# Kernel tuning notes

Measured on AMD Instinct MI355X. Metric: run time of the kernel, lower is better.

The kernel has to match this reference:

```python
import jax, jax.numpy as jnp
import numpy as np

N_NODES = 20000
N_EDGES = 320000
N_FEAT = 128
N_CLASS = 10
NEG_SLOPE = 0.2  # PyG GATConv default LeakyReLU slope


def gat_conv(x, src, dst, ew, W, a_src, a_dst, b, heads, ch, concat):
    """PyG-style GATConv with multiplicative edge_weight on messages.
    x: [N, Fin]; src/dst: [E] (self-loops already included); ew: [E].
    """
    N = x.shape[0]
    h = (x @ W).reshape(N, heads, ch)                      # [N,H,C]
    al_s = jnp.sum(h * a_src, axis=-1)                     # [N,H]
    al_d = jnp.sum(h * a_dst, axis=-1)                     # [N,H]
    e = jax.nn.leaky_relu(al_s[src] + al_d[dst], NEG_SLOPE)  # [E,H]
    # segment softmax over incoming edges of each target node
    m = jax.ops.segment_max(e, dst, num_segments=N)        # [N,H]
    ex = jnp.exp(e - m[dst])
    den = jax.ops.segment_sum(ex, dst, num_segments=N)     # [N,H]
    alpha = ex / (den[dst] + 1e-16)                        # [E,H]
    msg = h[src] * (alpha * ew[:, None])[..., None]        # [E,H,C]
    out = jax.ops.segment_sum(msg, dst, num_segments=N)    # [N,H,C]
    out = out.reshape(N, heads * ch) if concat else out.mean(axis=1)
    return out + b


def setup_inputs() -> dict:
    key = jax.random.key(0)
    ks = jax.random.split(key, 20)
    d = {}
    d["x"] = jax.random.normal(ks[0], (N_NODES, N_FEAT), dtype=jnp.float32)
    d["edge_index"] = jax.random.randint(ks[1], (2, N_EDGES), 0, N_NODES, dtype=jnp.int32)
    d["edge_weight"] = jnp.ones((N_EDGES,), dtype=jnp.float32)

    def glorot(k, shape):
        fan = shape[0] + shape[-1]
        return jax.random.uniform(k, shape, jnp.float32, -1.0, 1.0) * np.sqrt(6.0 / fan)

    H1, C1 = 4, 256
    H3, C3 = 6, N_CLASS
    d["W1"] = glorot(ks[2], (N_FEAT, H1 * C1))
    d["a1s"] = glorot(ks[3], (H1, C1)) * 0.1
    d["a1d"] = glorot(ks[4], (H1, C1)) * 0.1
    d["b1"] = jnp.zeros((H1 * C1,), jnp.float32)
    d["lw1"] = glorot(ks[5], (N_FEAT, H1 * C1))
    d["lb1"] = jnp.zeros((H1 * C1,), jnp.float32)

    d["W2"] = glorot(ks[6], (H1 * C1, H1 * C1))
    d["a2s"] = glorot(ks[7], (H1, C1)) * 0.1
    d["a2d"] = glorot(ks[8], (H1, C1)) * 0.1
    d["b2"] = jnp.zeros((H1 * C1,), jnp.float32)
    d["lw2"] = glorot(ks[9], (H1 * C1, H1 * C1))
    d["lb2"] = jnp.zeros((H1 * C1,), jnp.float32)

    d["W3"] = glorot(ks[10], (H1 * C1, H3 * C3))
    d["a3s"] = glorot(ks[11], (H3, C3)) * 0.1
    d["a3d"] = glorot(ks[12], (H3, C3)) * 0.1
    d["b3"] = jnp.zeros((C3,), jnp.float32)
    d["lw3"] = glorot(ks[13], (H1 * C1, C3))
    d["lb3"] = jnp.zeros((C3,), jnp.float32)
    return d


def reference(x, edge_index, edge_weight,
              W1, a1s, a1d, b1, lw1, lb1,
              W2, a2s, a2d, b2, lw2, lb2,
              W3, a3s, a3d, b3, lw3, lb3):
    N = x.shape[0]
    # PyG GATConv adds self-loops (fill edge_weight with 1.0)
    loop = jnp.arange(N, dtype=edge_index.dtype)
    src = jnp.concatenate([edge_index[0], loop])
    dst = jnp.concatenate([edge_index[1], loop])
    ew = jnp.concatenate([edge_weight, jnp.ones((N,), edge_weight.dtype)])

    h = jax.nn.elu(gat_conv(x, src, dst, ew, W1, a1s, a1d, b1, 4, 256, True)
                   + (x @ lw1 + lb1))
    h = jax.nn.elu(gat_conv(h, src, dst, ew, W2, a2s, a2d, b2, 4, 256, True)
                   + (h @ lw2 + lb2))
    out = gat_conv(h, src, dst, ew, W3, a3s, a3d, b3, 6, N_CLASS, False) \
          + (h @ lw3 + lb3)
    return out
```

## Files before the change

### kernel.cpp

```cpp
#include <hip/hip_runtime.h>

typedef __attribute__((ext_vector_type(8))) short s16x8;
typedef __attribute__((ext_vector_type(8))) __bf16 bf16x8;
typedef __attribute__((ext_vector_type(4))) float f32x4;

__device__ inline float bf2f(ushort u){ return __uint_as_float(((unsigned)u)<<16); }
__device__ inline ushort f2bf(float f){
  unsigned u = __float_as_uint(f);
  unsigned r = (u + 0x7fffu + ((u>>16)&1u)) >> 16;
  return (ushort)r;
}

__device__ inline void gl_lds16(const ushort* g, ushort* l){
  __builtin_amdgcn_global_load_lds(
      (const __attribute__((address_space(1))) unsigned int*)g,
      (__attribute__((address_space(3))) unsigned int*)l,
      16, 0, 0);
}

__global__ void k_count(const int* __restrict__ ei, int* __restrict__ counts,
                        int E, int ET){
  int e = blockIdx.x*256 + threadIdx.x;
  if (e >= ET) return;
  int dst = (e < E) ? ei[E + e] : (e - E);
  atomicAdd(&counts[dst], 1);
}

__global__ __launch_bounds__(1024) void k_scan(const int* __restrict__ cnt,
                                               int* __restrict__ indptr, int N){
  __shared__ int part[1024];
  int t = threadIdx.x;
  int per = (N + 1023) / 1024;
  int base = t * per;
  int s = 0;
  for (int i = 0; i < per; ++i){ int idx = base + i; if (idx < N) s += cnt[idx]; }
  part[t] = s; __syncthreads();
  for (int off = 1; off < 1024; off <<= 1){
    int v = (t >= off) ? part[t-off] : 0;
    __syncthreads();
    if (t >= off) part[t] += v;
    __syncthreads();
  }
  int run = (t == 0) ? 0 : part[t-1];
  for (int i = 0; i < per; ++i){
    int idx = base + i;
    if (idx < N){ indptr[idx] = run; run += cnt[idx]; }
  }
  if (t == 1023) indptr[N] = run;
}

__global__ void k_fill(const int* __restrict__ ei, const float* __restrict__ ew,
                       const int* __restrict__ indptr, int* __restrict__ cursor,
                       int* __restrict__ csrc, float* __restrict__ cew,
                       int E, int ET){
  int e = blockIdx.x*256 + threadIdx.x;
  if (e >= ET) return;
  int src, dst; float w;
  if (e < E){ src = ei[e]; dst = ei[E + e]; w = ew[e]; }
  else { src = dst = e - E; w = 1.0f; }
  int pos = indptr[dst] + atomicAdd(&cursor[dst], 1);
  csrc[pos] = src; cew[pos] = w;
}

__global__ void k_f2b(const float* __restrict__ x, ushort* __restrict__ xb,
                      int n8valid, int n8total){
  int i = blockIdx.x*256 + threadIdx.x;
  if (i >= n8total) return;
  s16x8 o = {0,0,0,0,0,0,0,0};
  if (i < n8valid){
    const float4* p = (const float4*)x + (size_t)i*2;
    float4 a = p[0], b = p[1];
    o[0]=(short)f2bf(a.x); o[1]=(short)f2bf(a.y); o[2]=(short)f2bf(a.z); o[3]=(short)f2bf(a.w);
    o[4]=(short)f2bf(b.x); o[5]=(short)f2bf(b.y); o[6]=(short)f2bf(b.z); o[7]=(short)f2bf(b.w);
  }
  *((s16x8*)xb + i) = o;
}

__global__ __launch_bounds__(256) void k_packB(
    const float* __restrict__ W, const float* __restrict__ LW,
    ushort* __restrict__ BT, int K, int NW, int NL, int Npad)
{
  __shared__ float tile[32][33];
  int k0 = blockIdx.x*32, n0 = blockIdx.y*32;
  int c = threadIdx.x & 31, r4 = threadIdx.x >> 5;
  #pragma unroll
  for (int rr = 0; rr < 32; rr += 8){
    int k = k0 + r4 + rr, n = n0 + c;
    float v = 0.f;
    if (k < K){
      if (n < NW)            v = W[(size_t)k*NW + n];
      else if (n < NW + NL)  v = LW[(size_t)k*NL + (n - NW)];
    }
    tile[r4+rr][c] = v;
  }
  __syncthreads();
  #pragma unroll
  for (int rr = 0; rr < 32; rr += 8){
    int n = n0 + r4 + rr, k = k0 + c;
    if (n < Npad && k < K) BT[(size_t)n*K + k] = f2bf(tile[c][r4+rr]);
  }
}

__global__ __launch_bounds__(256) void k_gemm(
    const ushort* __restrict__ A, const ushort* __restrict__ BT,
    ushort* __restrict__ Gatt, ushort* __restrict__ Skip,
    int K, int GW, int SW, int NCB, int CPX)
{
  __shared__ ushort As[128*64];
  __shared__ ushort Bs[128*64];
  const int bid = blockIdx.x;
  const int lb = CPX ? ((bid & 7)*CPX + (bid >> 3)) : bid;
  const size_t row0 = (size_t)(lb / NCB) * 128;
  const size_t col0 = (size_t)(lb % NCB) * 128;
  const int t = threadIdx.x;
  const int l = t & 63, w = t >> 6;
  const int wr = w >> 1, wc = w & 1;
  const int sr = l >> 3;
  const int sk = ((l & 7) ^ sr) << 3;
  const ushort* gA = A  + (row0 + w*8 + sr)*(size_t)K + sk;
  const ushort* gB = BT + (col0 + w*8 + sr)*(size_t)K + sk;
  ushort* lA = As + w*512;
  ushort* lB = Bs + w*512;
  const int rf = l & 15;
  const int g4 = l >> 4;
  f32x4 acc[4][4] = {};

  for (int k0 = 0; k0 < K; k0 += 64){
    #pragma unroll
    for (int i = 0; i < 4; ++i){
      gl_lds16(gA + k0 + (size_t)(i*32)*K, lA + i*2048);
      gl_lds16(gB + k0 + (size_t)(i*32)*K, lB + i*2048);
    }
    __syncthreads();
    #pragma unroll
    for (int kk = 0; kk < 2; ++kk){
      const int koff = ((((kk<<2) | g4) ^ (rf & 7)) << 3);
      bf16x8 af[4], bfr[4];
      #pragma unroll
      for (int i = 0; i < 4; ++i)
        af[i] = __builtin_bit_cast(bf16x8, *(const s16x8*)(As + (wr*64 + i*16 + rf)*64 + koff));
      #pragma unroll
      for (int j = 0; j < 4; ++j)
        bfr[j] = __builtin_bit_cast(bf16x8, *(const s16x8*)(Bs + (wc*64 + j*16 + rf)*64 + koff));
      #pragma unroll
      for (int i = 0; i < 4; ++i)
        #pragma unroll
        for (int j = 0; j < 4; ++j)
          acc[i][j] = __builtin_amdgcn_mfma_f32_16x16x32_bf16(af[i], bfr[j], acc[i][j], 0, 0, 0);
    }
    __syncthreads();
  }

  #pragma unroll
  for (int i = 0; i < 4; ++i){
    #pragma unroll
    for (int j = 0; j < 4; ++j){
      int gc = (int)col0 + wc*64 + j*16 + rf;
      #pragma unroll
      for (int r = 0; r < 4; ++r){
        size_t gr = row0 + wr*64 + i*16 + (g4<<2) + r;
        float v = acc[i][j][r];
        if (gc < GW)            Gatt[gr*GW + gc] = f2bf(v);
        else if (gc < GW + SW)  Skip[gr*SW + (gc - GW)] = f2bf(v);
      }
    }
  }
}

#define STG8(p0, hh, ktv, offU) do { \
  const ushort* _g = (p0) + (((size_t)(hh))<<7)*(size_t)K + (((size_t)(ktv))<<6); \
  gl_lds16(_g, S + (offU) + (w<<9)); \
  gl_lds16(_g + ((size_t)K<<6), S + (offU) + 4096 + (w<<9)); \
} while(0)

#define RD_A(base_) do { _Pragma("unroll") \
  for (int i_ = 0; i_ < 4; ++i_){ \
    const int hr = wr*64 + i_*16 + rf; const int sw = hr & 7; \
    av[i_][0] = *(const bf16x8*)((base_) + hr*64 + ((g4 ^ sw) << 3)); \
    av[i_][1] = *(const bf16x8*)((base_) + hr*64 + (((4|g4) ^ sw) << 3)); } \
} while(0)

#define RD_B(base_, dst_) do { _Pragma("unroll") \
  for (int j_ = 0; j_ < 2; ++j_){ \
    const int cf = wc*32 + j_*16 + rf; const int sw = cf & 7; \
    dst_[j_][0] = *(const bf16x8*)((base_) + cf*64 + ((g4 ^ sw) << 3)); \
    dst_[j_][1] = *(const bf16x8*)((base_) + cf*64 + (((4|g4) ^ sw) << 3)); } \
} while(0)

#define MM8(mh, nh, bv_) do { \
  __builtin_amdgcn_s_setprio(1); \
  _Pragma("unroll") \
  for (int kk_ = 0; kk_ < 2; ++kk_) \
    _Pragma("unroll") \
    for (int i_ = 0; i_ < 4; ++i_) \
      _Pragma("unroll") \
      for (int j_ = 0; j_ < 2; ++j_) \
        acc[mh][nh][i_][j_] = __builtin_amdgcn_mfma_f32_16x16x32_bf16( \
            av[i_][kk_], bv_[j_][kk_], acc[mh][nh][i_][j_], 0, 0, 0); \
  __builtin_amdgcn_s_setprio(0); \
} while(0)

__global__ __launch_bounds__(512, 1) void k_gemm8(
    const ushort* __restrict__ A, const ushort* __restrict__ BT,
    ushort* __restrict__ Gatt, ushort* __restrict__ Skip,
    int K, int GW, int CPX)
{
  __shared__ ushort S[65536];
  const int bid = blockIdx.x;
  const int lb = (bid & 7)*CPX + (bid >> 3);
  const size_t row0 = (size_t)(lb >> 3) * 256;
  const size_t col0 = (size_t)(lb & 7) * 256;
  const int t = threadIdx.x;
  const int l = t & 63, w = t >> 6;
  const int wr = w >> 2, wc = w & 3;
  const int rf = l & 15, g4 = l >> 4;
  const int T = K >> 6;

  const int r0 = t >> 3, s0 = t & 7;
  const ushort* pA = A  + (row0 + r0)*(size_t)K + ((s0 ^ (r0 & 7)) << 3);
  const ushort* pB = BT + (col0 + r0)*(size_t)K + ((s0 ^ (r0 & 7)) << 3);

  f32x4 acc[2][2][4][2] = {};
  bf16x8 av[4][2], bvlo[2][2], bvhi[2][2];

  STG8(pA, 0, 0, 0);
  STG8(pB, 0, 0, 16384);
  STG8(pA, 1, 0, 8192);
  STG8(pB, 1, 0, 24576);
  STG8(pA, 0, 1, 32768);
  STG8(pB, 0, 1, 49152);
  asm volatile("s_waitcnt vmcnt(4)");
  asm volatile("s_barrier" ::: "memory");

  for (int u = 0; u < T; ++u){
    const int b = u & 1;
    const int bbase = b << 15;
    const int nbase = bbase ^ 32768;
    const bool un1 = (u + 1 < T), un2 = (u + 2 < T);
    const ushort* Alo = S + bbase;
    const ushort* Ahi = S + bbase + 8192;
    const ushort* Blo = S + bbase + 16384;
    const ushort* Bhi = S + bbase + 24576;
    RD_A(Alo); RD_B(Blo, bvlo);
    if (un1) STG8(pA, 1, u+1, nbase + 8192);
    MM8(0, 0, bvlo);
    asm volatile("s_barrier" ::: "memory");
    RD_B(Bhi, bvhi);
    if (un1) STG8(pB, 1, u+1, nbase + 24576);
    MM8(0, 1, bvhi);
    asm volatile("s_barrier" ::: "memory");
    RD_A(Ahi);
    if (un2) STG8(pA, 0, u+2, bbase);
    MM8(1, 1, bvhi);
    asm volatile("s_barrier" ::: "memory");
    if (un2) STG8(pB, 0, u+2, bbase + 16384);
    MM8(1, 0, bvlo);
    if (un2) asm volatile("s_waitcnt vmcnt(4)");
    else     asm volatile("s_waitcnt vmcnt(0)");
    asm volatile("s_barrier" ::: "memory");
  }

  ushort* outp; int cb;
  if ((int)col0 < GW){ outp = Gatt; cb = (int)col0; }
  else               { outp = Skip; cb = (int)col0 - GW; }
  #pragma unroll
  for (int mh = 0; mh < 2; ++mh)
    #pragma unroll
    for (int i = 0; i < 4; ++i)
      #pragma unroll
      for (int rr = 0; rr < 4; ++rr){
        size_t gr = row0 + mh*128 + wr*64 + i*16 + (g4<<2) + rr;
        ushort* rp = outp + gr*1024 + cb;
        #pragma unroll
        for (int nh = 0; nh < 2; ++nh)
          #pragma unroll
          for (int j = 0; j < 2; ++j)
            rp[nh*128 + wc*32 + j*16 + rf] = f2bf(acc[mh][nh][i][j][rr]);
      }
}

__global__ __launch_bounds__(256) void k_al(const ushort* __restrict__ Gatt,
    const float* __restrict__ a_s, const float* __restrict__ a_d,
    float* __restrict__ als, float* __restrict__ ald, int N){
  int gw = (blockIdx.x*blockDim.x + threadIdx.x) >> 6;
  int l = threadIdx.x & 63;
  if (gw >= N) return;
  const ushort* row = Gatt + (size_t)gw*1024;
  int c0 = l*16;
  s16x8 v0 = *(const s16x8*)(row + c0);
  s16x8 v1 = *(const s16x8*)(row + c0 + 8);
  float ps = 0.f, pd = 0.f;
  #pragma unroll
  for (int q = 0; q < 8; ++q){
    float f0 = bf2f((ushort)v0[q]), f1 = bf2f((ushort)v1[q]);
    ps += f0*a_s[c0+q] + f1*a_s[c0+8+q];
    pd += f0*a_d[c0+q] + f1*a_d[c0+8+q];
  }
  #pragma unroll
  for (int off = 8; off; off >>= 1){
    ps += __shfl_down(ps, off);
    pd += __shfl_down(pd, off);
  }
  if ((l & 15) == 0){
    als[(size_t)gw*4 + (l>>4)] = ps;
    ald[(size_t)gw*4 + (l>>4)] = pd;
  }
}

__global__ __launch_bounds__(256) void k_agg(
    const ushort* __restrict__ Gatt,
    const ushort* __restrict__ Skip,
    const float*  __restrict__ als,
    const float*  __restrict__ ald,
    const float*  __restrict__ bias,
    const float*  __restrict__ lbias,
    const int*    __restrict__ indptr,
    const int*    __restrict__ csrc,
    const float*  __restrict__ cew,
    ushort* __restrict__ Hout,
    int N)
{
  const int t = threadIdx.x;
  const int l = t & 63, w = t >> 6;
  const int n = blockIdx.x*4 + w;
  const int h2 = l >> 4;
  const int col = l*16;
  if (n >= N){
    s16x8 z = {0,0,0,0,0,0,0,0};
    *(s16x8*)(Hout + (size_t)n*1024 + col)     = z;
    *(s16x8*)(Hout + (size_t)n*1024 + col + 8) = z;
    return;
  }
  const int beg = indptr[n];
  const int deg = indptr[n+1] - beg;
  const int hh = l & 3;
  const float aldh = ald[(size_t)n*4 + hh];

  float m = -1e30f, d = 0.f;
  for (int c0 = 0; c0 < deg; c0 += 16){
    int i = c0 + (l >> 2);
    bool act = (i < deg);
    float e = -1e30f;
    if (act){
      int s = csrc[beg + i];
      float r_ = als[(size_t)s*4 + hh] + aldh;
      e = r_ > 0.f ? r_ : 0.2f*r_;
    }
    float cm = e;
    #pragma unroll
    for (int o = 4; o < 64; o <<= 1) cm = fmaxf(cm, __shfl_xor(cm, o));
    float nm = fmaxf(m, cm);
    float ex = act ? __expf(e - nm) : 0.f;
    #pragma unroll
    for (int o = 4; o < 64; o <<= 1) ex += __shfl_xor(ex, o);
    d = d * __expf(m - nm) + ex;
    m = nm;
  }
  d += 1e-16f;
  const float inv_d = 1.0f / d;

  float a[16];
  #pragma unroll
  for (int q = 0; q < 16; ++q) a[q] = 0.f;
  const ushort* gbase = Gatt + col;
  for (int c0 = 0; c0 < deg; c0 += 16){
    int i = c0 + (l >> 2);
    int nc = min(16, deg - c0);
    float wv = 0.f; int sv = 0;
    if (i < deg){
      sv = csrc[beg + i];
      float r_ = als[(size_t)sv*4 + hh] + aldh;
      float e = r_ > 0.f ? r_ : 0.2f*r_;
      wv = __expf(e - m) * inv_d * cew[beg + i];
    }
    for (int jj = 0; jj < nc; ++jj){
      float wg = __shfl(wv, (jj << 2) | h2);
      int s    = __shfl(sv, jj << 2);
      const ushort* rp = gbase + (size_t)s*1024;
      s16x8 h0 = *(const s16x8*)rp;
      s16x8 h1 = *(const s16x8*)(rp + 8);
      #pragma unroll
      for (int q = 0; q < 8; ++q) a[q]   += wg * bf2f((ushort)h0[q]);
      #pragma unroll
      for (int q = 0; q < 8; ++q) a[q+8] += wg * bf2f((ushort)h1[q]);
    }
  }

  s16x8 sk0 = *(const s16x8*)(Skip + (size_t)n*1024 + col);
  s16x8 sk1 = *(const s16x8*)(Skip + (size_t)n*1024 + col + 8);
  s16x8 ov0, ov1;
  #pragma unroll
  for (int q = 0; q < 8; ++q){
    float v = a[q] + bias[col+q] + lbias[col+q] + bf2f((ushort)sk0[q]);
    v = v > 0.f ? v : __expf(v) - 1.f;
    ov0[q] = (short)f2bf(v);
    float v2 = a[q+8] + bias[col+8+q] + lbias[col+8+q] + bf2f((ushort)sk1[q]);
    v2 = v2 > 0.f ? v2 : __expf(v2) - 1.f;
    ov1[q] = (short)f2bf(v2);
  }
  *(s16x8*)(Hout + (size_t)n*1024 + col)     = ov0;
  *(s16x8*)(Hout + (size_t)n*1024 + col + 8) = ov1;
}

__global__ void k_al3(const ushort* __restrict__ G3, const float* __restrict__ a_s,
                      const float* __restrict__ a_d,
                      float* __restrict__ als, float* __restrict__ ald, int N){
  int n = blockIdx.x*256 + threadIdx.x;
  if (n >= N) return;
  const ushort* row = G3 + (size_t)n*60;
  #pragma unroll
  for (int h = 0; h < 6; ++h){
    float ps = 0.f, pd = 0.f;
    #pragma unroll
    for (int c = 0; c < 10; ++c){
      float v = bf2f(row[h*10 + c]);
      ps += v * a_s[h*10 + c];
      pd += v * a_d[h*10 + c];
    }
    als[(size_t)n*6 + h] = ps;
    ald[(size_t)n*6 + h] = pd;
  }
}

__global__ __launch_bounds__(64) void k_agg3(
    const ushort* __restrict__ G3,
    const ushort* __restrict__ Skip3,
    const float*  __restrict__ als,
    const float*  __restrict__ ald,
    const float*  __restrict__ b3,
    const float*  __restrict__ lb3,
    const int*    __restrict__ indptr,
    const int*    __restrict__ csrc,
    const float*  __restrict__ cew,
    float* __restrict__ out, int N)
{
  const int n = blockIdx.x;
  const int l = threadIdx.x;
  const int beg = indptr[n], deg = indptr[n+1] - beg;
  __shared__ float s_aldh[6];
  __shared__ int   s_src[64];
  __shared__ float s_wgt[64][6];
  __shared__ float s_o[6][10];
  if (l < 6) s_aldh[l] = ald[(size_t)n*6 + l];
  __syncthreads();
  float m0=-1e30f,m1=-1e30f,m2=-1e30f,m3=-1e30f,m4=-1e30f,m5=-1e30f;
  float d0=0.f,d1=0.f,d2=0.f,d3=0.f,d4=0.f,d5=0.f;
  for (int c0 = 0; c0 < deg; c0 += 64){
    int nc = min(64, deg - c0);
    bool act = l < nc;
    int s = act ? csrc[beg + c0 + l] : 0;
#define HP(hh, mm, dd) { \
    float e = -1e30f; \
    if (act){ float r_ = als[(size_t)s*6 + hh] + s_aldh[hh]; e = r_ > 0.f ? r_ : 0.2f*r_; } \
    float cm = e; \
    for (int o_ = 32; o_; o_ >>= 1) cm = fmaxf(cm, __shfl_xor(cm, o_)); \
    float nm = fmaxf(mm, cm); \
    float ex = act ? __expf(e - nm) : 0.f; \
    for (int o_ = 32; o_; o_ >>= 1) ex += __shfl_xor(ex, o_); \
    dd = dd * __expf(mm - nm) + ex; mm = nm; }
    HP(0,m0,d0) HP(1,m1,d1) HP(2,m2,d2) HP(3,m3,d3) HP(4,m4,d4) HP(5,m5,d5)
#undef HP
  }
  const int h = l / 10, c = l % 10;
  float o = 0.f;
  for (int c0 = 0; c0 < deg; c0 += 64){
    int nc = min(64, deg - c0);
    if (l < nc){
      int s = csrc[beg + c0 + l];
      s_src[l] = s;
      float w_ = cew[beg + c0 + l];
#define WP(hh, mm, dd) { \
      float r_ = als[(size_t)s*6 + hh] + s_aldh[hh]; \
      float e = r_ > 0.f ? r_ : 0.2f*r_; \
      s_wgt[l][hh] = __expf(e - mm) / (dd + 1e-16f) * w_; }
      WP(0,m0,d0) WP(1,m1,d1) WP(2,m2,d2) WP(3,m3,d3) WP(4,m4,d4) WP(5,m5,d5)
#undef WP
    }
    __syncthreads();
    if (l < 60){
      for (int i = 0; i < nc; ++i)
        o += s_wgt[i][h] * bf2f(G3[(size_t)s_src[i]*60 + l]);
    }
    __syncthreads();
  }
  if (l < 60) s_o[h][c] = o;
  __syncthreads();
  if (l < 10){
    float v = (s_o[0][l]+s_o[1][l]+s_o[2][l]+s_o[3][l]+s_o[4][l]+s_o[5][l]) * (1.0f/6.0f);
    v += b3[l] + lb3[l] + bf2f(Skip3[(size_t)n*10 + l]);
    out[(size_t)n*10 + l] = v;
  }
}

extern "C" void kernel_launch(void* const* d_in, const int* in_sizes, int n_in,
                              void* d_out, int out_size, void* d_ws, size_t ws_size,
                              hipStream_t stream)
{
  const int N = 20000, F = 128, E = 320000, ET = E + N;
  const int Mpad = 20224;
  const int F1 = 1024, NT = 2048;
  const int NWG1 = (Mpad/128)*(NT/128);
  const int NWG2 = (Mpad/256)*(NT/256);

  const float* x   = (const float*)d_in[0];
  const int*   ei  = (const int*)  d_in[1];
  const float* ew  = (const float*)d_in[2];
  const float* W1  = (const float*)d_in[3];
  const float* a1s = (const float*)d_in[4];
  const float* a1d = (const float*)d_in[5];
  const float* b1  = (const float*)d_in[6];
  const float* lw1 = (const float*)d_in[7];
  const float* lb1 = (const float*)d_in[8];
  const float* W2  = (const float*)d_in[9];
  const float* a2s = (const float*)d_in[10];
  const float* a2d = (const float*)d_in[11];
  const float* b2  = (const float*)d_in[12];
  const float* lw2 = (const float*)d_in[13];
  const float* lb2 = (const float*)d_in[14];
  const float* W3  = (const float*)d_in[15];
  const float* a3s = (const float*)d_in[16];
  const float* a3d = (const float*)d_in[17];
  const float* b3  = (const float*)d_in[18];
  const float* lw3 = (const float*)d_in[19];
  const float* lb3 = (const float*)d_in[20];

  char* ws = (char*)d_ws;
  size_t off = 0;
  auto alloc = [&](size_t bytes) -> void* {
    void* p = ws + off;
    off = (off + bytes + 255) & ~(size_t)255;
    return p;
  };
  ushort* Gatt = (ushort*)alloc((size_t)Mpad*F1*2);
  ushort* Skip = (ushort*)alloc((size_t)Mpad*F1*2);
  ushort* H    = (ushort*)alloc((size_t)Mpad*F1*2);
  ushort* xb   = (ushort*)alloc((size_t)Mpad*F*2);
  ushort* BT   = (ushort*)alloc((size_t)NT*1024*2);
  float*  als  = (float*) alloc((size_t)N*6*4);
  float*  ald  = (float*) alloc((size_t)N*6*4);
  int*    counts = (int*)alloc((size_t)2*N*4);
  int*    cursor = counts + N;
  int*    indptr = (int*)alloc((size_t)(N+1)*4);
  int*    csrc   = (int*)alloc((size_t)ET*4);
  float*  cew    = (float*)alloc((size_t)ET*4);
  if (off > ws_size) return;

  hipMemsetAsync(counts, 0, (size_t)2*N*4, stream);
  k_count<<<(ET+255)/256, 256, 0, stream>>>(ei, counts, E, ET);
  k_scan<<<1, 1024, 0, stream>>>(counts, indptr, N);
  k_fill<<<(ET+255)/256, 256, 0, stream>>>(ei, ew, indptr, cursor, csrc, cew, E, ET);
  k_f2b<<<(Mpad*F/8+255)/256, 256, 0, stream>>>(x, xb, N*F/8, Mpad*F/8);

  k_packB<<<dim3((F+31)/32, NT/32), 256, 0, stream>>>(W1, lw1, BT, F, 1024, 1024, NT);
  k_gemm<<<dim3(NWG1), 256, 0, stream>>>(xb, BT, Gatt, Skip, F, 1024, 1024, NT/128, NWG1/8);
  k_al<<<(N+3)/4, 256, 0, stream>>>(Gatt, a1s, a1d, als, ald, N);
  k_agg<<<Mpad/4, 256, 0, stream>>>(Gatt, Skip, als, ald, b1, lb1, indptr, csrc, cew, H, N);

  k_packB<<<dim3(F1/32, NT/32), 256, 0, stream>>>(W2, lw2, BT, F1, 1024, 1024, NT);
  k_gemm8<<<dim3(NWG2), 512, 0, stream>>>(H, BT, Gatt, Skip, F1, 1024, NWG2/8);
  k_al<<<(N+3)/4, 256, 0, stream>>>(Gatt, a2s, a2d, als, ald, N);
  k_agg<<<Mpad/4, 256, 0, stream>>>(Gatt, Skip, als, ald, b2, lb2, indptr, csrc, cew, H, N);

  k_packB<<<dim3(F1/32, 128/32), 256, 0, stream>>>(W3, lw3, BT, F1, 60, 10, 128);
  k_gemm<<<dim3(Mpad/128), 256, 0, stream>>>(H, BT, Gatt, Skip, F1, 60, 10, 1, 0);
  k_al3<<<(N+255)/256, 256, 0, stream>>>(Gatt, a3s, a3d, als, ald, N);
  k_agg3<<<N, 64, 0, stream>>>(Gatt, Skip, als, ald, b3, lb3, indptr, csrc, cew,
                               (float*)d_out, N);
}
```

Measured before the change: 501.6 us.

## Merge prep kernels, batch weight packing, split-K layer-3 GEMM, unroll aggregation

Folds the edge-count and x-to-bf16 conversion into one launch, and packs all three weight matrices in a single launch into separate buffers. Layer 1 now runs on the large-tile k_gemm8 kernel (K=128) instead of the small-tile GEMM. The narrow layer-3 GEMM is split four ways along K into fp32 partials that a new reduction kernel sums. The k_gemm8 main loop is peeled so the final two steps carry no conditionals, and the aggregation gather handles two neighbours per iteration for more loads in flight. The cost is an extra fp32 partial buffer and reduction pass, plus possible poor fit of the 256-tile GEMM at K=128 (only two K steps).

After: 480.7 us. 1.04x faster.

```diff
diff --git a/kernel.cpp b/kernel.cpp
--- a/kernel.cpp
+++ b/kernel.cpp
@@ -18,12 +18,27 @@
       16, 0, 0);
 }
 
-__global__ void k_count(const int* __restrict__ ei, int* __restrict__ counts,
-                        int E, int ET){
-  int e = blockIdx.x*256 + threadIdx.x;
-  if (e >= ET) return;
-  int dst = (e < E) ? ei[E + e] : (e - E);
-  atomicAdd(&counts[dst], 1);
+__global__ void k_prep(const int* __restrict__ ei, int* __restrict__ counts,
+                       const float* __restrict__ x, ushort* __restrict__ xb,
+                       int E, int ET, int ETb, int n8valid, int n8total){
+  int b = blockIdx.x;
+  if (b < ETb){
+    int e = b*256 + threadIdx.x;
+    if (e >= ET) return;
+    int dst = (e < E) ? ei[E + e] : (e - E);
+    atomicAdd(&counts[dst], 1);
+  } else {
+    int i = (b - ETb)*256 + threadIdx.x;
+    if (i >= n8total) return;
+    s16x8 o = {0,0,0,0,0,0,0,0};
+    if (i < n8valid){
+      const float4* p = (const float4*)x + (size_t)i*2;
+      float4 a = p[0], bb = p[1];
+      o[0]=(short)f2bf(a.x); o[1]=(short)f2bf(a.y); o[2]=(short)f2bf(a.z); o[3]=(short)f2bf(a.w);
+      o[4]=(short)f2bf(bb.x); o[5]=(short)f2bf(bb.y); o[6]=(short)f2bf(bb.z); o[7]=(short)f2bf(bb.w);
+    }
+    *((s16x8*)xb + i) = o;
+  }
 }
 
 __global__ __launch_bounds__(1024) void k_scan(const int* __restrict__ cnt,
@@ -62,26 +77,18 @@
   csrc[pos] = src; cew[pos] = w;
 }
 
-__global__ void k_f2b(const float* __restrict__ x, ushort* __restrict__ xb,
-                      int n8valid, int n8total){
-  int i = blockIdx.x*256 + threadIdx.x;
-  if (i >= n8total) return;
-  s16x8 o = {0,0,0,0,0,0,0,0};
-  if (i < n8valid){
-    const float4* p = (const float4*)x + (size_t)i*2;
-    float4 a = p[0], b = p[1];
-    o[0]=(short)f2bf(a.x); o[1]=(short)f2bf(a.y); o[2]=(short)f2bf(a.z); o[3]=(short)f2bf(a.w);
-    o[4]=(short)f2bf(b.x); o[5]=(short)f2bf(b.y); o[6]=(short)f2bf(b.z); o[7]=(short)f2bf(b.w);
-  }
-  *((s16x8*)xb + i) = o;
-}
-
-__global__ __launch_bounds__(256) void k_packB(
-    const float* __restrict__ W, const float* __restrict__ LW,
-    ushort* __restrict__ BT, int K, int NW, int NL, int Npad)
+__global__ __launch_bounds__(256) void k_packB3(
+    const float* __restrict__ W1, const float* __restrict__ Lw1, ushort* __restrict__ B1,
+    const float* __restrict__ W2, const float* __restrict__ Lw2, ushort* __restrict__ B2,
+    const float* __restrict__ W3, const float* __restrict__ Lw3, ushort* __restrict__ B3)
 {
   __shared__ float tile[32][33];
-  int k0 = blockIdx.x*32, n0 = blockIdx.y*32;
+  int b = blockIdx.x;
+  const float *W, *L; ushort* B; int K, NW, NL, Np, nkb, lb;
+  if (b < 256)      { W=W1; L=Lw1; B=B1; K=128;  NW=1024; NL=1024; Np=2048; nkb=4;  lb=b; }
+  else if (b < 2304){ W=W2; L=Lw2; B=B2; K=1024; NW=1024; NL=1024; Np=2048; nkb=32; lb=b-256; }
+  else              { W=W3; L=Lw3; B=B3; K=1024; NW=60;   NL=10;   Np=128;  nkb=32; lb=b-2304; }
+  int k0 = (lb % nkb)*32, n0 = (lb / nkb)*32;
   int c = threadIdx.x & 31, r4 = threadIdx.x >> 5;
   #pragma unroll
   for (int rr = 0; rr < 32; rr += 8){
@@ -89,7 +96,7 @@
     float v = 0.f;
     if (k < K){
       if (n < NW)            v = W[(size_t)k*NW + n];
-      else if (n < NW + NL)  v = LW[(size_t)k*NL + (n - NW)];
+      else if (n < NW + NL)  v = L[(size_t)k*NL + (n - NW)];
     }
     tile[r4+rr][c] = v;
   }
@@ -97,35 +104,35 @@
   #pragma unroll
   for (int rr = 0; rr < 32; rr += 8){
     int n = n0 + r4 + rr, k = k0 + c;
-    if (n < Npad && k < K) BT[(size_t)n*K + k] = f2bf(tile[c][r4+rr]);
-  }
-}
-
-__global__ __launch_bounds__(256) void k_gemm(
+    if (n < Np && k < K) B[(size_t)n*K + k] = f2bf(tile[c][r4+rr]);
+  }
+}
+
+__global__ __launch_bounds__(256) void k_gemm_sk(
     const ushort* __restrict__ A, const ushort* __restrict__ BT,
-    ushort* __restrict__ Gatt, ushort* __restrict__ Skip,
-    int K, int GW, int SW, int NCB, int CPX)
+    float* __restrict__ P, int K, int kseg, int Mpad)
 {
   __shared__ ushort As[128*64];
   __shared__ ushort Bs[128*64];
   const int bid = blockIdx.x;
-  const int lb = CPX ? ((bid & 7)*CPX + (bid >> 3)) : bid;
-  const size_t row0 = (size_t)(lb / NCB) * 128;
-  const size_t col0 = (size_t)(lb % NCB) * 128;
+  const int part = bid & 3;
+  const size_t row0 = (size_t)(bid >> 2) * 128;
+  const int kbeg = part * kseg;
+  const int kend = kbeg + kseg;
   const int t = threadIdx.x;
   const int l = t & 63, w = t >> 6;
   const int wr = w >> 1, wc = w & 1;
   const int sr = l >> 3;
   const int sk = ((l & 7) ^ sr) << 3;
   const ushort* gA = A  + (row0 + w*8 + sr)*(size_t)K + sk;
-  const ushort* gB = BT + (col0 + w*8 + sr)*(size_t)K + sk;
+  const ushort* gB = BT + (w*8 + sr)*(size_t)K + sk;
   ushort* lA = As + w*512;
   ushort* lB = Bs + w*512;
   const int rf = l & 15;
   const int g4 = l >> 4;
   f32x4 acc[4][4] = {};
 
-  for (int k0 = 0; k0 < K; k0 += 64){
+  for (int k0 = kbeg; k0 < kend; k0 += 64){
     #pragma unroll
     for (int i = 0; i < 4; ++i){
       gl_lds16(gA + k0 + (size_t)(i*32)*K, lA + i*2048);
@@ -151,20 +158,30 @@
     __syncthreads();
   }
 
+  float* Pp = P + (size_t)part * Mpad * 128;
   #pragma unroll
   for (int i = 0; i < 4; ++i){
     #pragma unroll
     for (int j = 0; j < 4; ++j){
-      int gc = (int)col0 + wc*64 + j*16 + rf;
+      int gc = wc*64 + j*16 + rf;
       #pragma unroll
       for (int r = 0; r < 4; ++r){
         size_t gr = row0 + wr*64 + i*16 + (g4<<2) + r;
-        float v = acc[i][j][r];
-        if (gc < GW)            Gatt[gr*GW + gc] = f2bf(v);
-        else if (gc < GW + SW)  Skip[gr*SW + (gc - GW)] = f2bf(v);
+        Pp[gr*128 + gc] = acc[i][j][r];
       }
     }
   }
+}
+
+__global__ void k_red3(const float* __restrict__ P, ushort* __restrict__ G3,
+                       ushort* __restrict__ S3, int Mpad){
+  int idx = blockIdx.x*256 + threadIdx.x;
+  int row = idx >> 7, gc = idx & 127;
+  if (row >= Mpad || gc >= 70) return;
+  const size_t st = (size_t)Mpad*128;
+  float v = P[idx] + P[idx+st] + P[idx+2*st] + P[idx+3*st];
+  if (gc < 60) G3[(size_t)row*60 + gc] = f2bf(v);
+  else         S3[(size_t)row*10 + (gc-60)] = f2bf(v);
 }
 
 #define STG8(p0, hh, ktv, offU) do { \
@@ -198,6 +215,33 @@
         acc[mh][nh][i_][j_] = __builtin_amdgcn_mfma_f32_16x16x32_bf16( \
             av[i_][kk_], bv_[j_][kk_], acc[mh][nh][i_][j_], 0, 0, 0); \
   __builtin_amdgcn_s_setprio(0); \
+} while(0)
+
+#define KSTEP(u_, UN1, UN2) do { \
+  const int b_ = (u_) & 1; \
+  const int bbase = b_ << 15; \
+  const int nbase = bbase ^ 32768; \
+  const ushort* Alo = S + bbase; \
+  const ushort* Ahi = S + bbase + 8192; \
+  const ushort* Blo = S + bbase + 16384; \
+  const ushort* Bhi = S + bbase + 24576; \
+  RD_A(Alo); RD_B(Blo, bvlo); \
+  if (UN1) STG8(pA, 1, (u_)+1, nbase + 8192); \
+  MM8(0, 0, bvlo); \
+  asm volatile("s_barrier" ::: "memory"); \
+  RD_B(Bhi, bvhi); \
+  if (UN1) STG8(pB, 1, (u_)+1, nbase + 24576); \
+  MM8(0, 1, bvhi); \
+  asm volatile("s_barrier" ::: "memory"); \
+  RD_A(Ahi); \
+  if (UN2) STG8(pA, 0, (u_)+2, bbase); \
+  MM8(1, 1, bvhi); \
+  asm volatile("s_barrier" ::: "memory"); \
+  if (UN2) STG8(pB, 0, (u_)+2, bbase + 16384); \
+  MM8(1, 0, bvlo); \
+  if (UN2) asm volatile("s_waitcnt vmcnt(4)"); \
+  else     asm volatile("s_waitcnt vmcnt(0)"); \
+  asm volatile("s_barrier" ::: "memory"); \
 } while(0)
 
 __global__ __launch_bounds__(512, 1) void k_gemm8(
@@ -232,33 +276,10 @@
   asm volatile("s_waitcnt vmcnt(4)");
   asm volatile("s_barrier" ::: "memory");
 
-  for (int u = 0; u < T; ++u){
-    const int b = u & 1;
-    const int bbase = b << 15;
-    const int nbase = bbase ^ 32768;
-    const bool un1 = (u + 1 < T), un2 = (u + 2 < T);
-    const ushort* Alo = S + bbase;
-    const ushort* Ahi = S + bbase + 8192;
-    const ushort* Blo = S + bbase + 16384;
-    const ushort* Bhi = S + bbase + 24576;
-    RD_A(Alo); RD_B(Blo, bvlo);
-    if (un1) STG8(pA, 1, u+1, nbase + 8192);
-    MM8(0, 0, bvlo);
-    asm volatile("s_barrier" ::: "memory");
-    RD_B(Bhi, bvhi);
-    if (un1) STG8(pB, 1, u+1, nbase + 24576);
-    MM8(0, 1, bvhi);
-    asm volatile("s_barrier" ::: "memory");
-    RD_A(Ahi);
-    if (un2) STG8(pA, 0, u+2, bbase);
-    MM8(1, 1, bvhi);
-    asm volatile("s_barrier" ::: "memory");
-    if (un2) STG8(pB, 0, u+2, bbase + 16384);
-    MM8(1, 0, bvlo);
-    if (un2) asm volatile("s_waitcnt vmcnt(4)");
-    else     asm volatile("s_waitcnt vmcnt(0)");
-    asm volatile("s_barrier" ::: "memory");
-  }
+  int u = 0;
+  for (; u + 2 < T; ++u) KSTEP(u, true, true);
+  KSTEP(u, true, false); ++u;
+  KSTEP(u, false, false);
 
   ushort* outp; int cb;
   if ((int)col0 < GW){ outp = Gatt; cb = (int)col0; }
@@ -373,16 +394,35 @@
       float e = r_ > 0.f ? r_ : 0.2f*r_;
       wv = __expf(e - m) * inv_d * cew[beg + i];
     }
-    for (int jj = 0; jj < nc; ++jj){
+    int jj = 0;
+    for (; jj + 1 < nc; jj += 2){
+      float wg0 = __shfl(wv, (jj << 2) | h2);
+      int   sg0 = __shfl(sv, jj << 2);
+      float wg1 = __shfl(wv, ((jj+1) << 2) | h2);
+      int   sg1 = __shfl(sv, (jj+1) << 2);
+      const ushort* rp0 = gbase + (size_t)sg0*1024;
+      const ushort* rp1 = gbase + (size_t)sg1*1024;
+      s16x8 x0 = *(const s16x8*)rp0;
+      s16x8 x1 = *(const s16x8*)(rp0 + 8);
+      s16x8 y0 = *(const s16x8*)rp1;
+      s16x8 y1 = *(const s16x8*)(rp1 + 8);
+      #pragma unroll
+      for (int q = 0; q < 8; ++q){
+        a[q]   += wg0 * bf2f((ushort)x0[q]) + wg1 * bf2f((ushort)y0[q]);
+        a[q+8] += wg0 * bf2f((ushort)x1[q]) + wg1 * bf2f((ushort)y1[q]);
+      }
+    }
+    if (jj < nc){
       float wg = __shfl(wv, (jj << 2) | h2);
-      int s    = __shfl(sv, jj << 2);
+      int   s  = __shfl(sv, jj << 2);
       const ushort* rp = gbase + (size_t)s*1024;
       s16x8 h0 = *(const s16x8*)rp;
       s16x8 h1 = *(const s16x8*)(rp + 8);
       #pragma unroll
-      for (int q = 0; q < 8; ++q) a[q]   += wg * bf2f((ushort)h0[q]);
-      #pragma unroll
-      for (int q = 0; q < 8; ++q) a[q+8] += wg * bf2f((ushort)h1[q]);
+      for (int q = 0; q < 8; ++q){
+        a[q]   += wg * bf2f((ushort)h0[q]);
+        a[q+8] += wg * bf2f((ushort)h1[q]);
+      }
     }
   }
 
@@ -499,7 +539,6 @@
   const int N = 20000, F = 128, E = 320000, ET = E + N;
   const int Mpad = 20224;
   const int F1 = 1024, NT = 2048;
-  const int NWG1 = (Mpad/128)*(NT/128);
   const int NWG2 = (Mpad/256)*(NT/256);
 
   const float* x   = (const float*)d_in[0];
@@ -535,7 +574,10 @@
   ushort* Skip = (ushort*)alloc((size_t)Mpad*F1*2);
   ushort* H    = (ushort*)alloc((size_t)Mpad*F1*2);
   ushort* xb   = (ushort*)alloc((size_t)Mpad*F*2);
-  ushort* BT   = (ushort*)alloc((size_t)NT*1024*2);
+  ushort* BT1  = (ushort*)alloc((size_t)NT*F*2);
+  ushort* BT2  = (ushort*)alloc((size_t)NT*F1*2);
+  ushort* BT3  = (ushort*)alloc((size_t)128*F1*2);
+  float*  P    = (float*) alloc((size_t)4*Mpad*128*4);
   float*  als  = (float*) alloc((size_t)N*6*4);
   float*  ald  = (float*) alloc((size_t)N*6*4);
   int*    counts = (int*)alloc((size_t)2*N*4);
@@ -545,24 +587,26 @@
   float*  cew    = (float*)alloc((size_t)ET*4);
   if (off > ws_size) return;
 
+  const int ETb = (ET + 255)/256;
+  const int n8tot = Mpad*F/8;
+  const int n8b = (n8tot + 255)/256;
+
   hipMemsetAsync(counts, 0, (size_t)2*N*4, stream);
-  k_count<<<(ET+255)/256, 256, 0, stream>>>(ei, counts, E, ET);
+  k_prep<<<ETb + n8b, 256, 0, stream>>>(ei, counts, x, xb, E, ET, ETb, N*F/8, n8tot);
   k_scan<<<1, 1024, 0, stream>>>(counts, indptr, N);
   k_fill<<<(ET+255)/256, 256, 0, stream>>>(ei, ew, indptr, cursor, csrc, cew, E, ET);
-  k_f2b<<<(Mpad*F/8+255)/256, 256, 0, stream>>>(x, xb, N*F/8, Mpad*F/8);
-
-  k_packB<<<dim3((F+31)/32, NT/32), 256, 0, stream>>>(W1, lw1, BT, F, 1024, 1024, NT);
-  k_gemm<<<dim3(NWG1), 256, 0, stream>>>(xb, BT, Gatt, Skip, F, 1024, 1024, NT/128, NWG1/8);
+  k_packB3<<<2432, 256, 0, stream>>>(W1, lw1, BT1, W2, lw2, BT2, W3, lw3, BT3);
+
+  k_gemm8<<<dim3(NWG2), 512, 0, stream>>>(xb, BT1, Gatt, Skip, F, 1024, NWG2/8);
   k_al<<<(N+3)/4, 256, 0, stream>>>(Gatt, a1s, a1d, als, ald, N);
   k_agg<<<Mpad/4, 256, 0, stream>>>(Gatt, Skip, als, ald, b1, lb1, indptr, csrc, cew, H, N);
 
-  k_packB<<<dim3(F1/32, NT/32), 256, 0, stream>>>(W2, lw2, BT, F1, 1024, 1024, NT);
-  k_gemm8<<<dim3(NWG2), 512, 0, stream>>>(H, BT, Gatt, Skip, F1, 1024, NWG2/8);
+  k_gemm8<<<dim3(NWG2), 512, 0, stream>>>(H, BT2, Gatt, Skip, F1, 1024, NWG2/8);
   k_al<<<(N+3)/4, 256, 0, stream>>>(Gatt, a2s, a2d, als, ald, N);
   k_agg<<<Mpad/4, 256, 0, stream>>>(Gatt, Skip, als, ald, b2, lb2, indptr, csrc, cew, H, N);
 
-  k_packB<<<dim3(F1/32, 128/32), 256, 0, stream>>>(W3, lw3, BT, F1, 60, 10, 128);
-  k_gemm<<<dim3(Mpad/128), 256, 0, stream>>>(H, BT, Gatt, Skip, F1, 60, 10, 1, 0);
+  k_gemm_sk<<<dim3((Mpad/128)*4), 256, 0, stream>>>(H, BT3, P, F1, F1/4, Mpad);
+  k_red3<<<(Mpad*128)/256, 256, 0, stream>>>(P, Gatt, Skip, Mpad);
   k_al3<<<(N+255)/256, 256, 0, stream>>>(Gatt, a3s, a3d, als, ald, N);
   k_agg3<<<N, 64, 0, stream>>>(Gatt, Skip, als, ald, b3, lb3, indptr, csrc, cew,
                                (float*)d_out, N);
```
